# Performance work log

Hardware: AMD Instinct MI355X
Metric: run time of the kernel (lower is better)

The kernel has to match this reference:

```python
import jax, jax.numpy as jnp
import numpy as np

B, S, NH, DM, REPR, FF = 256, 110, 12, 768, 1024, 3072
HD = DM // NH  # 64
LN_EPS = 1e-12


def setup_inputs() -> dict:
    key = jax.random.key(0)
    ks = jax.random.split(key, 20)
    s = 0.02
    inp = {
        'im_repr': jax.random.normal(ks[0], (B, REPR), jnp.float32),
        'q_repr':  jax.random.normal(ks[1], (B, S, DM), jnp.float32),
        # self-attention projections (768 -> 768)
        'Wq1': jax.random.normal(ks[2], (DM, DM), jnp.float32) * s,
        'bq1': jnp.zeros((DM,), jnp.float32),
        'Wk1': jax.random.normal(ks[3], (DM, DM), jnp.float32) * s,
        'bk1': jnp.zeros((DM,), jnp.float32),
        'Wv1': jax.random.normal(ks[4], (DM, DM), jnp.float32) * s,
        'bv1': jnp.zeros((DM,), jnp.float32),
        # cross-attention: query from 768, key/value from encoder width 1024
        'Wq2': jax.random.normal(ks[5], (DM, DM), jnp.float32) * s,
        'bq2': jnp.zeros((DM,), jnp.float32),
        'Wk2': jax.random.normal(ks[6], (REPR, DM), jnp.float32) * s,
        'bk2': jnp.zeros((DM,), jnp.float32),
        'Wv2': jax.random.normal(ks[7], (REPR, DM), jnp.float32) * s,
        'bv2': jnp.zeros((DM,), jnp.float32),
        # FFN (768 -> 3072 -> 768) + LayerNorm
        'W1': jax.random.normal(ks[8], (DM, FF), jnp.float32) * s,
        'b1': jnp.zeros((FF,), jnp.float32),
        'W2': jax.random.normal(ks[9], (FF, DM), jnp.float32) * s,
        'b2': jnp.zeros((DM,), jnp.float32),
        'ln_g': jnp.ones((DM,), jnp.float32),
        'ln_b': jnp.zeros((DM,), jnp.float32),
    }
    return inp


def _heads(x):
    # [B, L, DM] -> [B, NH, L, HD]
    b, l, _ = x.shape
    return x.reshape(b, l, NH, HD).transpose(0, 2, 1, 3)


def _attn(hq, hkv, Wq, bq, Wk, bk, Wv, bv):
    # scaled dot-product attention (the source's relative-position bias is dead
    # code: attention_scores is overwritten by a fresh QK^T before scaling)
    q = _heads(hq @ Wq + bq)      # [B,NH,Lq,HD]
    k = _heads(hkv @ Wk + bk)     # [B,NH,Lk,HD]
    v = _heads(hkv @ Wv + bv)
    scores = jnp.einsum('bhqd,bhkd->bhqk', q, k) / np.sqrt(HD).astype(np.float32)
    probs = jax.nn.softmax(scores, axis=-1)
    ctx = jnp.einsum('bhqk,bhkd->bhqd', probs, v)
    b, _, lq, _ = ctx.shape
    return ctx.transpose(0, 2, 1, 3).reshape(b, lq, DM)


def reference(im_repr, q_repr, Wq1, bq1, Wk1, bk1, Wv1, bv1,
              Wq2, bq2, Wk2, bk2, Wv2, bv2, W1, b1, W2, b2, ln_g, ln_b):
    # self-attention over query tokens
    q_attn = _attn(q_repr, q_repr, Wq1, bq1, Wk1, bk1, Wv1, bv1)
    # image representation broadcast across the S key/value positions
    vision = jnp.broadcast_to(im_repr[:, None, :], (B, S, REPR))
    x = _attn(q_attn, vision, Wq2, bq2, Wk2, bk2, Wv2, bv2).mean(axis=1)  # [B,DM]
    # FFN + residual + LayerNorm (dropout = identity in eval)
    h = jax.nn.gelu(x @ W1 + b1, approximate=False) @ W2 + b2
    y = x + h
    mu = y.mean(axis=-1, keepdims=True)
    var = ((y - mu) ** 2).mean(axis=-1, keepdims=True)
    return (y - mu) / jnp.sqrt(var + LN_EPS) * ln_g + ln_b
```

## Files before the change

kernel.cpp:

```cpp
#include <hip/hip_runtime.h>
#include <hip/hip_bf16.h>
#include <math.h>

#define BATCH 256
#define DM    768
#define REPR  1024
#define FF    3072

typedef __attribute__((ext_vector_type(8))) short bf16x8;
typedef __attribute__((ext_vector_type(4))) float f32x4;

__device__ __forceinline__ unsigned bf16rne(float f){
  union{float f; unsigned u;} x; x.f = f;
  return (x.u + 0x7FFFu + ((x.u >> 16) & 1u)) >> 16;
}
__device__ __forceinline__ unsigned pk2(float lo, float hi){
  return bf16rne(lo) | (bf16rne(hi) << 16);
}

__global__ __launch_bounds__(256)
void prep_g1(const float* __restrict__ Wv2, const float* __restrict__ W1,
             const float* __restrict__ W2, const float* __restrict__ im,
             ushort* __restrict__ W1t, ushort* __restrict__ W2t,
             float* __restrict__ P1)
{
  const int id = blockIdx.x, tid = threadIdx.x;

  if (id < 384) {
    const int z = id / 96, t2 = id % 96, bx = t2 % 12, by = t2 / 12;
    const int lane = tid & 63, wid = tid >> 6;
    const int wr = wid >> 1, wc = wid & 1;
    const int arow = by * 32 + wr * 16 + (lane & 15);
    const int colb = bx * 64 + wc * 32;
    const int kq8  = (lane >> 4) * 8;
    const int kb   = z * 256;

    const float* apf  = im + (size_t)arow * REPR + kb + kq8;
    const int c0 = colb + (lane & 15), c1 = c0 + 16;
    const float* wrow = Wv2 + (size_t)(kb + kq8) * DM;

    f32x4 acc0 = (f32x4)(0.0f), acc1 = (f32x4)(0.0f);

    float4 a0c = *(const float4*)apf, a1c = *(const float4*)(apf + 4);
    float b0c[8], b1c[8];
    #pragma unroll
    for (int j = 0; j < 8; ++j) {
      b0c[j] = wrow[(size_t)j * DM + c0];
      b1c[j] = wrow[(size_t)j * DM + c1];
    }

    for (int s = 0; s < 8; ++s) {
      float4 a0n, a1n; float b0n[8], b1n[8];
      const bool more = (s + 1) < 8;
      if (more) {
        const float* a2 = apf + (s + 1) * 32;
        a0n = *(const float4*)a2; a1n = *(const float4*)(a2 + 4);
        const float* w2r = wrow + (size_t)(s + 1) * 32 * DM;
        #pragma unroll
        for (int j = 0; j < 8; ++j) {
          b0n[j] = w2r[(size_t)j * DM + c0];
          b1n[j] = w2r[(size_t)j * DM + c1];
        }
      }
      union U { unsigned u[4]; bf16x8 v; } afr, bfr0, bfr1;
      afr.u[0] = pk2(a0c.x, a0c.y); afr.u[1] = pk2(a0c.z, a0c.w);
      afr.u[2] = pk2(a1c.x, a1c.y); afr.u[3] = pk2(a1c.z, a1c.w);
      #pragma unroll
      for (int j = 0; j < 4; ++j) {
        bfr0.u[j] = pk2(b0c[2*j], b0c[2*j+1]);
        bfr1.u[j] = pk2(b1c[2*j], b1c[2*j+1]);
      }
      acc0 = __builtin_amdgcn_mfma_f32_16x16x32_bf16(afr.v, bfr0.v, acc0, 0, 0, 0);
      acc1 = __builtin_amdgcn_mfma_f32_16x16x32_bf16(afr.v, bfr1.v, acc1, 0, 0, 0);
      if (more) {
        a0c = a0n; a1c = a1n;
        #pragma unroll
        for (int j = 0; j < 8; ++j) { b0c[j] = b0n[j]; b1c[j] = b1n[j]; }
      }
    }

    const int crow = by * 32 + wr * 16 + (lane >> 4) * 4;
    float* dst = P1 + (size_t)z * BATCH * DM;
    #pragma unroll
    for (int nf = 0; nf < 2; ++nf) {
      const int c = colb + nf * 16 + (lane & 15);
      const f32x4 a = nf ? acc1 : acc0;
      #pragma unroll
      for (int r = 0; r < 4; ++r)
        dst[(size_t)(crow + r) * DM + c] = a[r];
    }
    return;
  }

  const int rel0 = id - 384;
  const float* src; ushort* dst; int K, N, rel;
  if (rel0 < 576) { src = W1; dst = W1t; K = DM; N = FF; rel = rel0; }
  else            { src = W2; dst = W2t; K = FF; N = DM; rel = rel0 - 576; }
  const int ntk = K >> 6;
  const int k0 = (rel % ntk) * 64, n0 = (rel / ntk) * 64;

  __shared__ float lds[64][65];
  #pragma unroll
  for (int p = 0; p < 4; ++p) {
    const int r = p * 16 + (tid >> 4), c4 = (tid & 15) * 4;
    float4 v = *(const float4*)(src + (size_t)(k0 + r) * N + n0 + c4);
    lds[r][c4] = v.x; lds[r][c4+1] = v.y; lds[r][c4+2] = v.z; lds[r][c4+3] = v.w;
  }
  __syncthreads();
  #pragma unroll
  for (int p = 0; p < 4; ++p) {
    const int nn = p * 16 + (tid >> 4), k4 = (tid & 15) * 4;
    uint2 o = { pk2(lds[k4][nn], lds[k4+1][nn]),
                pk2(lds[k4+2][nn], lds[k4+3][nn]) };
    *(uint2*)(dst + (size_t)(n0 + nn) * K + k0 + k4) = o;
  }
}

__global__ __launch_bounds__(256)
void fixup_x(const float* __restrict__ P1, const float* __restrict__ bv2,
             float* __restrict__ xf, ushort* __restrict__ xbf)
{
  const int e = (blockIdx.x * 256 + threadIdx.x) * 4;
  const int c = e % DM;
  float4 s = *(const float4*)(P1 + e);
  #pragma unroll
  for (int z = 1; z < 4; ++z) {
    float4 v = *(const float4*)(P1 + (size_t)z * BATCH * DM + e);
    s.x += v.x; s.y += v.y; s.z += v.z; s.w += v.w;
  }
  float4 bb = *(const float4*)(bv2 + c);
  s.x += bb.x; s.y += bb.y; s.z += bb.z; s.w += bb.w;
  *(float4*)(xf + e) = s;
  uint2 o = { pk2(s.x, s.y), pk2(s.z, s.w) };
  *(uint2*)(xbf + e) = o;
}

template<int EPI>
__global__ __launch_bounds__(256)
void gemm_rr(const ushort* __restrict__ Abf, const ushort* __restrict__ Bt,
             const float* __restrict__ bias, float* __restrict__ outF,
             ushort* __restrict__ outH, int N, int K, int lda, int kcount)
{
  const int gx = gridDim.x, gy = gridDim.y;
  const int nwg = gx * gy;
  int id = blockIdx.y * gx + blockIdx.x;
  if ((nwg & 7) == 0) id = (id & 7) * (nwg >> 3) + (id >> 3);
  const int bx = id / gy, by = id % gy;

  const int lane = threadIdx.x & 63, wid = threadIdx.x >> 6;
  const int wr = wid >> 1, wc = wid & 1;
  const int arow = by * 32 + wr * 16 + (lane & 15);
  const int colb = bx * 64 + wc * 32;
  const int kq = (lane >> 4) * 8;
  const int kb = blockIdx.z * kcount;

  const ushort* ap  = Abf + (size_t)arow * lda + kb + kq;
  const ushort* bp0 = Bt + (size_t)(colb + (lane & 15)) * K + kb + kq;
  const ushort* bp1 = Bt + (size_t)(colb + 16 + (lane & 15)) * K + kb + kq;

  f32x4 acc0 = (f32x4)(0.0f), acc1 = (f32x4)(0.0f);
  const int nsteps = kcount >> 5;

  union U { uint4 q; bf16x8 v; };
  U a_c, b0_c, b1_c;
  a_c.q  = *(const uint4*)ap;
  b0_c.q = *(const uint4*)bp0;
  b1_c.q = *(const uint4*)bp1;

  for (int t = 0; t < nsteps; ++t) {
    U a_n, b0_n, b1_n;
    const bool more = (t + 1) < nsteps;
    if (more) {
      a_n.q  = *(const uint4*)(ap  + (t + 1) * 32);
      b0_n.q = *(const uint4*)(bp0 + (t + 1) * 32);
      b1_n.q = *(const uint4*)(bp1 + (t + 1) * 32);
    }
    acc0 = __builtin_amdgcn_mfma_f32_16x16x32_bf16(a_c.v, b0_c.v, acc0, 0, 0, 0);
    acc1 = __builtin_amdgcn_mfma_f32_16x16x32_bf16(a_c.v, b1_c.v, acc1, 0, 0, 0);
    if (more) { a_c = a_n; b0_c = b0_n; b1_c = b1_n; }
  }

  const int crow = by * 32 + wr * 16 + (lane >> 4) * 4;
  #pragma unroll
  for (int nf = 0; nf < 2; ++nf) {
    const int c = colb + nf * 16 + (lane & 15);
    const f32x4 a = nf ? acc1 : acc0;
    #pragma unroll
    for (int r = 0; r < 4; ++r) {
      const int row = crow + r;
      if (EPI == 0) {
        outF[(size_t)blockIdx.z * BATCH * N + (size_t)row * N + c] = a[r];
      } else {
        float v = a[r] + bias[c];
        v = 0.5f * v * (1.0f + erff(v * 0.70710678118654752f));
        outH[(size_t)row * N + c] = (ushort)bf16rne(v);
      }
    }
  }
}

__global__ __launch_bounds__(256)
void ln_final(const float* __restrict__ P3, const float* __restrict__ xf,
              const float* __restrict__ b2, const float* __restrict__ g,
              const float* __restrict__ be, float* __restrict__ out)
{
  const int row = blockIdx.x, tid = threadIdx.x;
  const int lane = tid & 63, wave = tid >> 6;

  float v[3];
  #pragma unroll
  for (int i = 0; i < 3; ++i) {
    const int c = tid + i * 256;
    float s = xf[(size_t)row * DM + c] + b2[c];
    #pragma unroll
    for (int z = 0; z < 8; ++z) s += P3[((size_t)z * BATCH + row) * DM + c];
    v[i] = s;
  }

  __shared__ float red[4];
  float s = v[0] + v[1] + v[2];
  #pragma unroll
  for (int o = 32; o > 0; o >>= 1) s += __shfl_down(s, o);
  if (lane == 0) red[wave] = s;
  __syncthreads();
  const float mu = (red[0] + red[1] + red[2] + red[3]) * (1.0f / 768.0f);
  __syncthreads();
  const float d0 = v[0] - mu, d1 = v[1] - mu, d2 = v[2] - mu;
  float q = d0*d0 + d1*d1 + d2*d2;
  #pragma unroll
  for (int o = 32; o > 0; o >>= 1) q += __shfl_down(q, o);
  if (lane == 0) red[wave] = q;
  __syncthreads();
  const float var = (red[0] + red[1] + red[2] + red[3]) * (1.0f / 768.0f);
  const float inv = rsqrtf(var + 1e-12f);

  float* o = out + (size_t)row * DM;
  o[tid      ] = d0 * inv * g[tid      ] + be[tid      ];
  o[tid + 256] = d1 * inv * g[tid + 256] + be[tid + 256];
  o[tid + 512] = d2 * inv * g[tid + 512] + be[tid + 512];
}

extern "C" void kernel_launch(void* const* d_in, const int* in_sizes, int n_in,
                              void* d_out, int out_size, void* d_ws, size_t ws_size,
                              hipStream_t stream)
{
  const float* im  = (const float*)d_in[0];
  const float* Wv2 = (const float*)d_in[12];
  const float* bv2 = (const float*)d_in[13];
  const float* W1  = (const float*)d_in[14];
  const float* b1  = (const float*)d_in[15];
  const float* W2  = (const float*)d_in[16];
  const float* b2  = (const float*)d_in[17];
  const float* g   = (const float*)d_in[18];
  const float* be  = (const float*)d_in[19];
  float* out = (float*)d_out;

  char* w = (char*)d_ws;
  ushort* W1t = (ushort*)(w);
  ushort* W2t = (ushort*)(w + 4718592);
  ushort* xbf = (ushort*)(w + 9437184);
  ushort* tbf = (ushort*)(w + 9830400);
  float*  xf  = (float*) (w + 11403264);
  float*  P1  = (float*) (w + 12189696);
  float*  P3  = (float*) (w + 15335424);

  prep_g1<<<1536, 256, 0, stream>>>(Wv2, W1, W2, im, W1t, W2t, P1);
  fixup_x<<<192, 256, 0, stream>>>(P1, bv2, xf, xbf);
  gemm_rr<1><<<dim3(48, 8, 1), 256, 0, stream>>>(xbf, W1t, b1, nullptr, tbf,
                                                 FF, DM, DM, 768);
  gemm_rr<0><<<dim3(12, 8, 8), 256, 0, stream>>>(tbf, W2t, nullptr, P3, nullptr,
                                                 DM, FF, FF, 384);
  ln_final<<<BATCH, 256, 0, stream>>>(P3, xf, b2, g, be, out);
}
```

Baseline: 54.43 us.

## Drop split-K for Wv2 projection and halve split-K in W2 GEMM

```diff
diff --git a/kernel.cpp b/kernel.cpp
--- a/kernel.cpp
+++ b/kernel.cpp
@@ -21,23 +21,23 @@
 __global__ __launch_bounds__(256)
 void prep_g1(const float* __restrict__ Wv2, const float* __restrict__ W1,
              const float* __restrict__ W2, const float* __restrict__ im,
+             const float* __restrict__ bv2,
              ushort* __restrict__ W1t, ushort* __restrict__ W2t,
-             float* __restrict__ P1)
+             float* __restrict__ xf, ushort* __restrict__ xbf)
 {
   const int id = blockIdx.x, tid = threadIdx.x;
 
-  if (id < 384) {
-    const int z = id / 96, t2 = id % 96, bx = t2 % 12, by = t2 / 12;
+  if (id < 96) {
+    const int bx = id % 12, by = id / 12;
     const int lane = tid & 63, wid = tid >> 6;
     const int wr = wid >> 1, wc = wid & 1;
     const int arow = by * 32 + wr * 16 + (lane & 15);
     const int colb = bx * 64 + wc * 32;
     const int kq8  = (lane >> 4) * 8;
-    const int kb   = z * 256;
-
-    const float* apf  = im + (size_t)arow * REPR + kb + kq8;
+
+    const float* apf  = im + (size_t)arow * REPR + kq8;
     const int c0 = colb + (lane & 15), c1 = c0 + 16;
-    const float* wrow = Wv2 + (size_t)(kb + kq8) * DM;
+    const float* wrow = Wv2 + (size_t)kq8 * DM;
 
     f32x4 acc0 = (f32x4)(0.0f), acc1 = (f32x4)(0.0f);
 
@@ -49,9 +49,9 @@
       b1c[j] = wrow[(size_t)j * DM + c1];
     }
 
-    for (int s = 0; s < 8; ++s) {
+    for (int s = 0; s < 32; ++s) {
       float4 a0n, a1n; float b0n[8], b1n[8];
-      const bool more = (s + 1) < 8;
+      const bool more = (s + 1) < 32;
       if (more) {
         const float* a2 = apf + (s + 1) * 32;
         a0n = *(const float4*)a2; a1n = *(const float4*)(a2 + 4);
@@ -80,19 +80,22 @@
     }
 
     const int crow = by * 32 + wr * 16 + (lane >> 4) * 4;
-    float* dst = P1 + (size_t)z * BATCH * DM;
     #pragma unroll
     for (int nf = 0; nf < 2; ++nf) {
       const int c = colb + nf * 16 + (lane & 15);
       const f32x4 a = nf ? acc1 : acc0;
+      const float bb = bv2[c];
       #pragma unroll
-      for (int r = 0; r < 4; ++r)
-        dst[(size_t)(crow + r) * DM + c] = a[r];
+      for (int r = 0; r < 4; ++r) {
+        const float v = a[r] + bb;
+        xf [(size_t)(crow + r) * DM + c] = v;
+        xbf[(size_t)(crow + r) * DM + c] = (ushort)bf16rne(v);
+      }
     }
     return;
   }
 
-  const int rel0 = id - 384;
+  const int rel0 = id - 96;
   const float* src; ushort* dst; int K, N, rel;
   if (rel0 < 576) { src = W1; dst = W1t; K = DM; N = FF; rel = rel0; }
   else            { src = W2; dst = W2t; K = FF; N = DM; rel = rel0 - 576; }
@@ -114,25 +117,6 @@
                 pk2(lds[k4+2][nn], lds[k4+3][nn]) };
     *(uint2*)(dst + (size_t)(n0 + nn) * K + k0 + k4) = o;
   }
-}
-
-__global__ __launch_bounds__(256)
-void fixup_x(const float* __restrict__ P1, const float* __restrict__ bv2,
-             float* __restrict__ xf, ushort* __restrict__ xbf)
-{
-  const int e = (blockIdx.x * 256 + threadIdx.x) * 4;
-  const int c = e % DM;
-  float4 s = *(const float4*)(P1 + e);
-  #pragma unroll
-  for (int z = 1; z < 4; ++z) {
-    float4 v = *(const float4*)(P1 + (size_t)z * BATCH * DM + e);
-    s.x += v.x; s.y += v.y; s.z += v.z; s.w += v.w;
-  }
-  float4 bb = *(const float4*)(bv2 + c);
-  s.x += bb.x; s.y += bb.y; s.z += bb.z; s.w += bb.w;
-  *(float4*)(xf + e) = s;
-  uint2 o = { pk2(s.x, s.y), pk2(s.z, s.w) };
-  *(uint2*)(xbf + e) = o;
 }
 
 template<int EPI>
@@ -213,7 +197,7 @@
     const int c = tid + i * 256;
     float s = xf[(size_t)row * DM + c] + b2[c];
     #pragma unroll
-    for (int z = 0; z < 8; ++z) s += P3[((size_t)z * BATCH + row) * DM + c];
+    for (int z = 0; z < 4; ++z) s += P3[((size_t)z * BATCH + row) * DM + c];
     v[i] = s;
   }
 
@@ -261,14 +245,12 @@
   ushort* xbf = (ushort*)(w + 9437184);
   ushort* tbf = (ushort*)(w + 9830400);
   float*  xf  = (float*) (w + 11403264);
-  float*  P1  = (float*) (w + 12189696);
-  float*  P3  = (float*) (w + 15335424);
-
-  prep_g1<<<1536, 256, 0, stream>>>(Wv2, W1, W2, im, W1t, W2t, P1);
-  fixup_x<<<192, 256, 0, stream>>>(P1, bv2, xf, xbf);
+  float*  P3  = (float*) (w + 12189696);
+
+  prep_g1<<<1248, 256, 0, stream>>>(Wv2, W1, W2, im, bv2, W1t, W2t, xf, xbf);
   gemm_rr<1><<<dim3(48, 8, 1), 256, 0, stream>>>(xbf, W1t, b1, nullptr, tbf,
                                                  FF, DM, DM, 768);
-  gemm_rr<0><<<dim3(12, 8, 8), 256, 0, stream>>>(tbf, W2t, nullptr, P3, nullptr,
-                                                 DM, FF, FF, 384);
+  gemm_rr<0><<<dim3(12, 8, 4), 256, 0, stream>>>(tbf, W2t, nullptr, P3, nullptr,
+                                                 DM, FF, FF, 768);
   ln_final<<<BATCH, 256, 0, stream>>>(P3, xf, b2, g, be, out);
 }
```

Result: slower. 66.50 us (+22.2%).

## Drop weight transpose pre-pass; read fp32 W1/W2 directly in GEMMs

Applied to the files above, without the earlier changes.

```diff
diff --git a/kernel.cpp b/kernel.cpp
--- a/kernel.cpp
+++ b/kernel.cpp
@@ -19,100 +19,70 @@
 }
 
 __global__ __launch_bounds__(256)
-void prep_g1(const float* __restrict__ Wv2, const float* __restrict__ W1,
-             const float* __restrict__ W2, const float* __restrict__ im,
-             ushort* __restrict__ W1t, ushort* __restrict__ W2t,
+void gemm_g1(const float* __restrict__ Wv2, const float* __restrict__ im,
              float* __restrict__ P1)
 {
-  const int id = blockIdx.x, tid = threadIdx.x;
-
-  if (id < 384) {
-    const int z = id / 96, t2 = id % 96, bx = t2 % 12, by = t2 / 12;
-    const int lane = tid & 63, wid = tid >> 6;
-    const int wr = wid >> 1, wc = wid & 1;
-    const int arow = by * 32 + wr * 16 + (lane & 15);
-    const int colb = bx * 64 + wc * 32;
-    const int kq8  = (lane >> 4) * 8;
-    const int kb   = z * 256;
-
-    const float* apf  = im + (size_t)arow * REPR + kb + kq8;
-    const int c0 = colb + (lane & 15), c1 = c0 + 16;
-    const float* wrow = Wv2 + (size_t)(kb + kq8) * DM;
-
-    f32x4 acc0 = (f32x4)(0.0f), acc1 = (f32x4)(0.0f);
-
-    float4 a0c = *(const float4*)apf, a1c = *(const float4*)(apf + 4);
-    float b0c[8], b1c[8];
-    #pragma unroll
-    for (int j = 0; j < 8; ++j) {
-      b0c[j] = wrow[(size_t)j * DM + c0];
-      b1c[j] = wrow[(size_t)j * DM + c1];
-    }
-
-    for (int s = 0; s < 8; ++s) {
-      float4 a0n, a1n; float b0n[8], b1n[8];
-      const bool more = (s + 1) < 8;
-      if (more) {
-        const float* a2 = apf + (s + 1) * 32;
-        a0n = *(const float4*)a2; a1n = *(const float4*)(a2 + 4);
-        const float* w2r = wrow + (size_t)(s + 1) * 32 * DM;
-        #pragma unroll
-        for (int j = 0; j < 8; ++j) {
-          b0n[j] = w2r[(size_t)j * DM + c0];
-          b1n[j] = w2r[(size_t)j * DM + c1];
-        }
+  const int z = blockIdx.z, bx = blockIdx.x, by = blockIdx.y;
+  const int tid = threadIdx.x;
+  const int lane = tid & 63, wid = tid >> 6;
+  const int wr = wid >> 1, wc = wid & 1;
+  const int arow = by * 32 + wr * 16 + (lane & 15);
+  const int colb = bx * 64 + wc * 32;
+  const int kq8  = (lane >> 4) * 8;
+  const int kb   = z * 256;
+
+  const float* apf  = im + (size_t)arow * REPR + kb + kq8;
+  const int c0 = colb + (lane & 15), c1 = c0 + 16;
+  const float* wrow = Wv2 + (size_t)(kb + kq8) * DM;
+
+  f32x4 acc0 = (f32x4)(0.0f), acc1 = (f32x4)(0.0f);
+  float4 a0c = *(const float4*)apf, a1c = *(const float4*)(apf + 4);
+  float b0c[8], b1c[8];
+  #pragma unroll
+  for (int j = 0; j < 8; ++j) {
+    b0c[j] = wrow[(size_t)j * DM + c0];
+    b1c[j] = wrow[(size_t)j * DM + c1];
+  }
+
+  for (int s = 0; s < 8; ++s) {
+    float4 a0n, a1n; float b0n[8], b1n[8];
+    const bool more = (s + 1) < 8;
+    if (more) {
+      const float* a2 = apf + (s + 1) * 32;
+      a0n = *(const float4*)a2; a1n = *(const float4*)(a2 + 4);
+      const float* w2r = wrow + (size_t)(s + 1) * 32 * DM;
+      #pragma unroll
+      for (int j = 0; j < 8; ++j) {
+        b0n[j] = w2r[(size_t)j * DM + c0];
+        b1n[j] = w2r[(size_t)j * DM + c1];
       }
-      union U { unsigned u[4]; bf16x8 v; } afr, bfr0, bfr1;
-      afr.u[0] = pk2(a0c.x, a0c.y); afr.u[1] = pk2(a0c.z, a0c.w);
-      afr.u[2] = pk2(a1c.x, a1c.y); afr.u[3] = pk2(a1c.z, a1c.w);
-      #pragma unroll
-      for (int j = 0; j < 4; ++j) {
-        bfr0.u[j] = pk2(b0c[2*j], b0c[2*j+1]);
-        bfr1.u[j] = pk2(b1c[2*j], b1c[2*j+1]);
-      }
-      acc0 = __builtin_amdgcn_mfma_f32_16x16x32_bf16(afr.v, bfr0.v, acc0, 0, 0, 0);
-      acc1 = __builtin_amdgcn_mfma_f32_16x16x32_bf16(afr.v, bfr1.v, acc1, 0, 0, 0);
-      if (more) {
-        a0c = a0n; a1c = a1n;
-        #pragma unroll
-        for (int j = 0; j < 8; ++j) { b0c[j] = b0n[j]; b1c[j] = b1n[j]; }
-      }
-    }
-
-    const int crow = by * 32 + wr * 16 + (lane >> 4) * 4;
-    float* dst = P1 + (size_t)z * BATCH * DM;
-    #pragma unroll
-    for (int nf = 0; nf < 2; ++nf) {
-      const int c = colb + nf * 16 + (lane & 15);
-      const f32x4 a = nf ? acc1 : acc0;
-      #pragma unroll
-      for (int r = 0; r < 4; ++r)
-        dst[(size_t)(crow + r) * DM + c] = a[r];
-    }
-    return;
-  }
-
-  const int rel0 = id - 384;
-  const float* src; ushort* dst; int K, N, rel;
-  if (rel0 < 576) { src = W1; dst = W1t; K = DM; N = FF; rel = rel0; }
-  else            { src = W2; dst = W2t; K = FF; N = DM; rel = rel0 - 576; }
-  const int ntk = K >> 6;
-  const int k0 = (rel % ntk) * 64, n0 = (rel / ntk) * 64;
-
-  __shared__ float lds[64][65];
-  #pragma unroll
-  for (int p = 0; p < 4; ++p) {
-    const int r = p * 16 + (tid >> 4), c4 = (tid & 15) * 4;
-    float4 v = *(const float4*)(src + (size_t)(k0 + r) * N + n0 + c4);
-    lds[r][c4] = v.x; lds[r][c4+1] = v.y; lds[r][c4+2] = v.z; lds[r][c4+3] = v.w;
-  }
-  __syncthreads();
-  #pragma unroll
-  for (int p = 0; p < 4; ++p) {
-    const int nn = p * 16 + (tid >> 4), k4 = (tid & 15) * 4;
-    uint2 o = { pk2(lds[k4][nn], lds[k4+1][nn]),
-                pk2(lds[k4+2][nn], lds[k4+3][nn]) };
-    *(uint2*)(dst + (size_t)(n0 + nn) * K + k0 + k4) = o;
+    }
+    union U { unsigned u[4]; bf16x8 v; } afr, bfr0, bfr1;
+    afr.u[0] = pk2(a0c.x, a0c.y); afr.u[1] = pk2(a0c.z, a0c.w);
+    afr.u[2] = pk2(a1c.x, a1c.y); afr.u[3] = pk2(a1c.z, a1c.w);
+    #pragma unroll
+    for (int j = 0; j < 4; ++j) {
+      bfr0.u[j] = pk2(b0c[2*j], b0c[2*j+1]);
+      bfr1.u[j] = pk2(b1c[2*j], b1c[2*j+1]);
+    }
+    acc0 = __builtin_amdgcn_mfma_f32_16x16x32_bf16(afr.v, bfr0.v, acc0, 0, 0, 0);
+    acc1 = __builtin_amdgcn_mfma_f32_16x16x32_bf16(afr.v, bfr1.v, acc1, 0, 0, 0);
+    if (more) {
+      a0c = a0n; a1c = a1n;
+      #pragma unroll
+      for (int j = 0; j < 8; ++j) { b0c[j] = b0n[j]; b1c[j] = b1n[j]; }
+    }
+  }
+
+  const int crow = by * 32 + wr * 16 + (lane >> 4) * 4;
+  float* dst = P1 + (size_t)z * BATCH * DM;
+  #pragma unroll
+  for (int nf = 0; nf < 2; ++nf) {
+    const int c = colb + nf * 16 + (lane & 15);
+    const f32x4 a = nf ? acc1 : acc0;
+    #pragma unroll
+    for (int r = 0; r < 4; ++r)
+      dst[(size_t)(crow + r) * DM + c] = a[r];
   }
 }
 
@@ -135,49 +105,60 @@
   *(uint2*)(xbf + e) = o;
 }
 
-template<int EPI>
-__global__ __launch_bounds__(256)
-void gemm_rr(const ushort* __restrict__ Abf, const ushort* __restrict__ Bt,
-             const float* __restrict__ bias, float* __restrict__ outF,
-             ushort* __restrict__ outH, int N, int K, int lda, int kcount)
-{
-  const int gx = gridDim.x, gy = gridDim.y;
-  const int nwg = gx * gy;
-  int id = blockIdx.y * gx + blockIdx.x;
-  if ((nwg & 7) == 0) id = (id & 7) * (nwg >> 3) + (id >> 3);
-  const int bx = id / gy, by = id % gy;
+__global__ __launch_bounds__(256)
+void gemm_g2(const ushort* __restrict__ xbf, const float* __restrict__ W1,
+             const float* __restrict__ b1, ushort* __restrict__ tbf)
+{
+  int id = blockIdx.y * 48 + blockIdx.x;
+  id = (id & 7) * 48 + (id >> 3);
+  const int bx = id / 8, by = id % 8;
 
   const int lane = threadIdx.x & 63, wid = threadIdx.x >> 6;
   const int wr = wid >> 1, wc = wid & 1;
   const int arow = by * 32 + wr * 16 + (lane & 15);
   const int colb = bx * 64 + wc * 32;
   const int kq = (lane >> 4) * 8;
-  const int kb = blockIdx.z * kcount;
-
-  const ushort* ap  = Abf + (size_t)arow * lda + kb + kq;
-  const ushort* bp0 = Bt + (size_t)(colb + (lane & 15)) * K + kb + kq;
-  const ushort* bp1 = Bt + (size_t)(colb + 16 + (lane & 15)) * K + kb + kq;
+
+  const ushort* ap = xbf + (size_t)arow * DM + kq;
+  const int c0 = colb + (lane & 15), c1 = c0 + 16;
+  const float* wrow = W1 + (size_t)kq * FF;
 
   f32x4 acc0 = (f32x4)(0.0f), acc1 = (f32x4)(0.0f);
-  const int nsteps = kcount >> 5;
-
   union U { uint4 q; bf16x8 v; };
-  U a_c, b0_c, b1_c;
-  a_c.q  = *(const uint4*)ap;
-  b0_c.q = *(const uint4*)bp0;
-  b1_c.q = *(const uint4*)bp1;
-
-  for (int t = 0; t < nsteps; ++t) {
-    U a_n, b0_n, b1_n;
-    const bool more = (t + 1) < nsteps;
-    if (more) {
-      a_n.q  = *(const uint4*)(ap  + (t + 1) * 32);
-      b0_n.q = *(const uint4*)(bp0 + (t + 1) * 32);
-      b1_n.q = *(const uint4*)(bp1 + (t + 1) * 32);
-    }
-    acc0 = __builtin_amdgcn_mfma_f32_16x16x32_bf16(a_c.v, b0_c.v, acc0, 0, 0, 0);
-    acc1 = __builtin_amdgcn_mfma_f32_16x16x32_bf16(a_c.v, b1_c.v, acc1, 0, 0, 0);
-    if (more) { a_c = a_n; b0_c = b0_n; b1_c = b1_n; }
+  U a_c;
+  a_c.q = *(const uint4*)ap;
+  float b0c[8], b1c[8];
+  #pragma unroll
+  for (int j = 0; j < 8; ++j) {
+    b0c[j] = wrow[(size_t)j * FF + c0];
+    b1c[j] = wrow[(size_t)j * FF + c1];
+  }
+
+  for (int t = 0; t < 24; ++t) {
+    U a_n; float b0n[8], b1n[8];
+    const bool more = (t + 1) < 24;
+    if (more) {
+      a_n.q = *(const uint4*)(ap + (t + 1) * 32);
+      const float* w2r = wrow + (size_t)(t + 1) * 32 * FF;
+      #pragma unroll
+      for (int j = 0; j < 8; ++j) {
+        b0n[j] = w2r[(size_t)j * FF + c0];
+        b1n[j] = w2r[(size_t)j * FF + c1];
+      }
+    }
+    union V { unsigned u[4]; bf16x8 v; } bfr0, bfr1;
+    #pragma unroll
+    for (int j = 0; j < 4; ++j) {
+      bfr0.u[j] = pk2(b0c[2*j], b0c[2*j+1]);
+      bfr1.u[j] = pk2(b1c[2*j], b1c[2*j+1]);
+    }
+    acc0 = __builtin_amdgcn_mfma_f32_16x16x32_bf16(a_c.v, bfr0.v, acc0, 0, 0, 0);
+    acc1 = __builtin_amdgcn_mfma_f32_16x16x32_bf16(a_c.v, bfr1.v, acc1, 0, 0, 0);
+    if (more) {
+      a_c = a_n;
+      #pragma unroll
+      for (int j = 0; j < 8; ++j) { b0c[j] = b0n[j]; b1c[j] = b1n[j]; }
+    }
   }
 
   const int crow = by * 32 + wr * 16 + (lane >> 4) * 4;
@@ -187,15 +168,79 @@
     const f32x4 a = nf ? acc1 : acc0;
     #pragma unroll
     for (int r = 0; r < 4; ++r) {
-      const int row = crow + r;
-      if (EPI == 0) {
-        outF[(size_t)blockIdx.z * BATCH * N + (size_t)row * N + c] = a[r];
-      } else {
-        float v = a[r] + bias[c];
-        v = 0.5f * v * (1.0f + erff(v * 0.70710678118654752f));
-        outH[(size_t)row * N + c] = (ushort)bf16rne(v);
+      float v = a[r] + b1[c];
+      v = 0.5f * v * (1.0f + erff(v * 0.70710678118654752f));
+      tbf[(size_t)(crow + r) * FF + c] = (ushort)bf16rne(v);
+    }
+  }
+}
+
+__global__ __launch_bounds__(256)
+void gemm_g3(const ushort* __restrict__ tbf, const float* __restrict__ W2,
+             float* __restrict__ P3)
+{
+  int id = blockIdx.y * 12 + blockIdx.x;
+  id = (id & 7) * 12 + (id >> 3);
+  const int bx = id / 8, by = id % 8;
+
+  const int lane = threadIdx.x & 63, wid = threadIdx.x >> 6;
+  const int wr = wid >> 1, wc = wid & 1;
+  const int arow = by * 32 + wr * 16 + (lane & 15);
+  const int colb = bx * 64 + wc * 32;
+  const int kq = (lane >> 4) * 8;
+  const int kb = blockIdx.z * 384;
+
+  const ushort* ap = tbf + (size_t)arow * FF + kb + kq;
+  const int c0 = colb + (lane & 15), c1 = c0 + 16;
+  const float* wrow = W2 + (size_t)(kb + kq) * DM;
+
+  f32x4 acc0 = (f32x4)(0.0f), acc1 = (f32x4)(0.0f);
+  union U { uint4 q; bf16x8 v; };
+  U a_c;
+  a_c.q = *(const uint4*)ap;
+  float b0c[8], b1c[8];
+  #pragma unroll
+  for (int j = 0; j < 8; ++j) {
+    b0c[j] = wrow[(size_t)j * DM + c0];
+    b1c[j] = wrow[(size_t)j * DM + c1];
+  }
+
+  for (int t = 0; t < 12; ++t) {
+    U a_n; float b0n[8], b1n[8];
+    const bool more = (t + 1) < 12;
+    if (more) {
+      a_n.q = *(const uint4*)(ap + (t + 1) * 32);
+      const float* w2r = wrow + (size_t)(t + 1) * 32 * DM;
+      #pragma unroll
+      for (int j = 0; j < 8; ++j) {
+        b0n[j] = w2r[(size_t)j * DM + c0];
+        b1n[j] = w2r[(size_t)j * DM + c1];
       }
     }
+    union V { unsigned u[4]; bf16x8 v; } bfr0, bfr1;
+    #pragma unroll
+    for (int j = 0; j < 4; ++j) {
+      bfr0.u[j] = pk2(b0c[2*j], b0c[2*j+1]);
+      bfr1.u[j] = pk2(b1c[2*j], b1c[2*j+1]);
+    }
+    acc0 = __builtin_amdgcn_mfma_f32_16x16x32_bf16(a_c.v, bfr0.v, acc0, 0, 0, 0);
+    acc1 = __builtin_amdgcn_mfma_f32_16x16x32_bf16(a_c.v, bfr1.v, acc1, 0, 0, 0);
+    if (more) {
+      a_c = a_n;
+      #pragma unroll
+      for (int j = 0; j < 8; ++j) { b0c[j] = b0n[j]; b1c[j] = b1n[j]; }
+    }
+  }
+
+  const int crow = by * 32 + wr * 16 + (lane >> 4) * 4;
+  float* dst = P3 + (size_t)blockIdx.z * BATCH * DM;
+  #pragma unroll
+  for (int nf = 0; nf < 2; ++nf) {
+    const int c = colb + nf * 16 + (lane & 15);
+    const f32x4 a = nf ? acc1 : acc0;
+    #pragma unroll
+    for (int r = 0; r < 4; ++r)
+      dst[(size_t)(crow + r) * DM + c] = a[r];
   }
 }
 
@@ -256,19 +301,15 @@
   float* out = (float*)d_out;
 
   char* w = (char*)d_ws;
-  ushort* W1t = (ushort*)(w);
-  ushort* W2t = (ushort*)(w + 4718592);
-  ushort* xbf = (ushort*)(w + 9437184);
-  ushort* tbf = (ushort*)(w + 9830400);
-  float*  xf  = (float*) (w + 11403264);
-  float*  P1  = (float*) (w + 12189696);
-  float*  P3  = (float*) (w + 15335424);
-
-  prep_g1<<<1536, 256, 0, stream>>>(Wv2, W1, W2, im, W1t, W2t, P1);
+  ushort* xbf = (ushort*)(w);
+  ushort* tbf = (ushort*)(w + 393216);
+  float*  xf  = (float*) (w + 1966080);
+  float*  P1  = (float*) (w + 2752512);
+  float*  P3  = (float*) (w + 5898240);
+
+  gemm_g1<<<dim3(12, 8, 4), 256, 0, stream>>>(Wv2, im, P1);
   fixup_x<<<192, 256, 0, stream>>>(P1, bv2, xf, xbf);
-  gemm_rr<1><<<dim3(48, 8, 1), 256, 0, stream>>>(xbf, W1t, b1, nullptr, tbf,
-                                                 FF, DM, DM, 768);
-  gemm_rr<0><<<dim3(12, 8, 8), 256, 0, stream>>>(tbf, W2t, nullptr, P3, nullptr,
-                                                 DM, FF, FF, 384);
+  gemm_g2<<<dim3(48, 8, 1), 256, 0, stream>>>(xbf, W1, b1, tbf);
+  gemm_g3<<<dim3(12, 8, 8), 256, 0, stream>>>(tbf, W2, P3);
   ln_final<<<BATCH, 256, 0, stream>>>(P3, xf, b2, g, be, out);
 }
```

Measured after the change: 44.88 us. 1.21x faster.
